# Kernel optimization log

Hardware: AMD Instinct MI355X
Metric: run time of the kernel (lower is better)

## Reference

```python
import jax, jax.numpy as jnp
import numpy as np

S, B, H = 4096, 64, 256
D = 2.0
SIGMA = D / 2.0


def setup_inputs() -> dict:
    key = jax.random.key(0)
    ks = jax.random.split(key, 7)
    return {
        "e": jax.random.normal(ks[0], (S, B, H), dtype=jnp.float32),
        "d": jax.random.normal(ks[1], (1, B, H), dtype=jnp.float32),
        "W_a": jax.random.normal(ks[2], (H, H), dtype=jnp.float32) / np.sqrt(H),
        "W_p": jax.random.normal(ks[3], (H, H), dtype=jnp.float32) / np.sqrt(H),
        "v_p": jax.random.normal(ks[4], (H, 1), dtype=jnp.float32) / np.sqrt(H),
        "lin_w": jax.random.normal(ks[5], (H, 2 * H), dtype=jnp.float32) / np.sqrt(2 * H),
        "lin_b": jax.random.normal(ks[6], (H,), dtype=jnp.float32) * 0.01,
    }


def reference(e, d, W_a, W_p, v_p, lin_w, lin_b):
    s = e.shape[0]
    # alignment: scores over source positions, softmax along S (dim 0 in torch)
    scores = jnp.sum((d @ W_a) * e, axis=2)          # [S, B]
    a = jax.nn.softmax(scores, axis=0)               # [S, B]
    # predictive position gating (Luong local-p attention)
    h = jnp.tanh(d[0] @ W_p)                         # [B, H]
    p_center = jax.nn.sigmoid((h @ v_p)[:, 0])[None, :] * s   # [1, B]
    pos = jnp.arange(s, dtype=e.dtype)[:, None]      # [S, 1]
    diff = p_center - pos                            # [S, B]
    mask = (jnp.abs(diff) <= D).astype(e.dtype)
    p = jnp.exp(-(diff * diff) / (2.0 * SIGMA * SIGMA)) * mask  # [S, B]
    w = a * p                                        # [S, B]
    context = jnp.einsum('sbh,sb->bh', e, w)[None]   # [1, B, H]
    x = jnp.concatenate([context, d], axis=2)        # [1, B, 2H]
    out = jax.nn.relu(x @ lin_w.T + lin_b)           # dropout = identity (eval)
    return out, w
```

## Files before the change

### kernel.cpp

```cpp
#include <hip/hip_runtime.h>
#include <math.h>

constexpr int S_ = 4096;
constexpr int B_ = 64;
constexpr int H_ = 256;
constexpr int NCH = 16;
constexpr int ROWS = S_ / NCH;
constexpr float SHIFT = 60.0f;


__global__ __launch_bounds__(256) void kMain(const float* __restrict__ e,
                                             const float* __restrict__ d,
                                             const float* __restrict__ W_a,
                                             float* __restrict__ dW,
                                             float* __restrict__ lpart,
                                             float* __restrict__ w_out) {
  const int bid = blockIdx.x;
  const int b = bid & 63;
  const int c = bid >> 6;
  const int t = threadIdx.x;
  const int w = t >> 6;
  const int lane = t & 63;

  __shared__ float4 part[4][64];
  __shared__ float4 dw4[64];
  __shared__ float lred[64];

  {
    const float* db = d + b * H_;
    const float4* Wa4 = (const float4*)W_a;
    float4 acc = make_float4(0.f, 0.f, 0.f, 0.f);
#pragma unroll 8
    for (int i = 0; i < 64; ++i) {
      const int k = w * 64 + i;
      const float dv = db[k];
      const float4 wa = Wa4[k * 64 + lane];
      acc.x = fmaf(dv, wa.x, acc.x);
      acc.y = fmaf(dv, wa.y, acc.y);
      acc.z = fmaf(dv, wa.z, acc.z);
      acc.w = fmaf(dv, wa.w, acc.w);
    }
    part[w][lane] = acc;
    __syncthreads();
    if (t < 64) {
      float4 a0 = part[0][t], a1 = part[1][t], a2 = part[2][t], a3 = part[3][t];
      float4 r = make_float4(a0.x + a1.x + a2.x + a3.x,
                             a0.y + a1.y + a2.y + a3.y,
                             a0.z + a1.z + a2.z + a3.z,
                             a0.w + a1.w + a2.w + a3.w);
      dw4[t] = r;
      if (c == 0) ((float4*)(dW + b * H_))[t] = r;
    }
    __syncthreads();
  }

  const int rr = lane >> 2;
  const int sub = lane & 3;
  float4 wreg[16];
#pragma unroll
  for (int j = 0; j < 16; ++j) wreg[j] = dw4[sub + 4 * j];

  float lsum = 0.f;
#pragma unroll 1
  for (int p = 0; p < 4; ++p) {
    const int s = c * ROWS + p * 64 + w * 16 + rr;
    const float4* erow = (const float4*)(e + ((size_t)s * B_ + b) * H_);
    float acc = 0.f;
#pragma unroll
    for (int half = 0; half < 2; ++half) {
      float4 ev[8];
#pragma unroll
      for (int j = 0; j < 8; ++j) ev[j] = erow[sub + 4 * (half * 8 + j)];
#pragma unroll
      for (int j = 0; j < 8; ++j) {
        const float4 wv = wreg[half * 8 + j];
        acc = fmaf(ev[j].x, wv.x, fmaf(ev[j].y, wv.y,
              fmaf(ev[j].z, wv.z, fmaf(ev[j].w, wv.w, acc))));
      }
    }
    acc += __shfl_xor(acc, 1, 64);
    acc += __shfl_xor(acc, 2, 64);
    if (sub == 0) lsum += expf(acc - SHIFT);
  }
  if (sub == 0) lred[w * 16 + rr] = lsum;
  __syncthreads();
  if (t < 64) {
    float v = lred[t];
#pragma unroll
    for (int off = 32; off > 0; off >>= 1) v += __shfl_xor(v, off, 64);
    if (t == 0) lpart[b * NCH + c] = v;
  }
  w_out[bid * 256 + t] = 0.f;
}

__global__ __launch_bounds__(1024) void kD(const float* __restrict__ e,
                                           const float* __restrict__ d,
                                           const float* __restrict__ W_p,
                                           const float* __restrict__ v_p,
                                           const float* __restrict__ lin_w,
                                           const float* __restrict__ lin_b,
                                           const float* __restrict__ dW,
                                           const float* __restrict__ lpart,
                                           float* __restrict__ out,
                                           float* __restrict__ w_out) {
  const int b = blockIdx.x;
  const int t = threadIdx.x;
  __shared__ float red[1024];
  __shared__ float sstate[2];
  __shared__ float scW[8];
  __shared__ float wsh[8];
  __shared__ float xbuf[512];

  {
    const int h = t & 255, kc = t >> 8;
    const float* db = d + b * H_;
    float ap = 0.f;
#pragma unroll 8
    for (int k = kc * 64; k < kc * 64 + 64; ++k)
      ap = fmaf(db[k], W_p[k * H_ + h], ap);
    red[t] = ap;
    __syncthreads();
    if (t < 256) {
      float sp = red[t] + red[t + 256] + red[t + 512] + red[t + 768];
      red[t] = tanhf(sp) * v_p[t];
    }
    __syncthreads();
    for (int st = 128; st > 0; st >>= 1) {
      if (t < st) red[t] += red[t + st];
      __syncthreads();
    }
    if (t == 0) {
      sstate[0] = (float)S_ / (1.f + expf(-red[0]));
      float L = 0.f;
#pragma unroll
      for (int j = 0; j < NCH; ++j) L += lpart[b * NCH + j];
      sstate[1] = 1.f / L;
    }
    __syncthreads();
  }
  const float pcb = sstate[0];
  const float invL = sstate[1];
  const int s0 = max(0, (int)ceilf(pcb - 2.f));
  const int s1 = min(S_ - 1, (int)floorf(pcb + 2.f));
  const int nw = s1 - s0 + 1;

  if (t < nw * 64) {
    const int j = t >> 6, lane = t & 63;
    const float4 ev = ((const float4*)(e + ((size_t)(s0 + j) * B_ + b) * H_))[lane];
    const float4 wv = ((const float4*)(dW + b * H_))[lane];
    float p = ev.x * wv.x + ev.y * wv.y + ev.z * wv.z + ev.w * wv.w;
#pragma unroll
    for (int off = 32; off > 0; off >>= 1) p += __shfl_xor(p, off, 64);
    if (lane == 0) scW[j] = p;
  }
  __syncthreads();
  if (t < nw) {
    const int s = s0 + t;
    const float diff = pcb - (float)s;
    const float wv = expf(scW[t] - SHIFT) * invL * expf(-0.5f * diff * diff);
    wsh[t] = wv;
    w_out[(size_t)s * B_ + b] = wv;
  }
  __syncthreads();
  if (t < 256) {
    float ctx = 0.f;
    for (int j = 0; j < nw; ++j)
      ctx = fmaf(wsh[j], e[((size_t)(s0 + j) * B_ + b) * H_ + t], ctx);
    xbuf[t] = ctx;
    xbuf[256 + t] = d[b * H_ + t];
  }
  __syncthreads();
  const int h = t >> 2, prt = t & 3;
  const float4* lw = (const float4*)(lin_w + h * 2 * H_) + prt * 32;
  const float4* xv = (const float4*)xbuf + prt * 32;
  float acc = 0.f;
#pragma unroll 8
  for (int k = 0; k < 32; ++k) {
    float4 a4 = lw[k], b4 = xv[k];
    acc += a4.x * b4.x + a4.y * b4.y + a4.z * b4.z + a4.w * b4.w;
  }
  red[t] = acc;
  __syncthreads();
  if (t < 256) {
    float r = red[4 * t] + red[4 * t + 1] + red[4 * t + 2] + red[4 * t + 3] + lin_b[t];
    out[b * H_ + t] = fmaxf(r, 0.f);
  }
}

extern "C" void kernel_launch(void* const* d_in, const int* in_sizes, int n_in,
                              void* d_out, int out_size, void* d_ws, size_t ws_size,
                              hipStream_t stream) {
  const float* e     = (const float*)d_in[0];
  const float* dd    = (const float*)d_in[1];
  const float* W_a   = (const float*)d_in[2];
  const float* W_p   = (const float*)d_in[3];
  const float* v_p   = (const float*)d_in[4];
  const float* lin_w = (const float*)d_in[5];
  const float* lin_b = (const float*)d_in[6];

  float* out   = (float*)d_out;
  float* w_out = out + B_ * H_;

  float* ws    = (float*)d_ws;
  float* dW    = ws;
  float* lpart = ws + 16384;

  kMain<<<B_ * NCH, 256, 0, stream>>>(e, dd, W_a, dW, lpart, w_out);
  kD<<<B_, 1024, 0, stream>>>(e, dd, W_p, v_p, lin_w, lin_b, dW, lpart, out, w_out);
}
```

Before: 69.67 us.

## Fuse the two kernels with a last-block-done atomic counter per batch

Merges the tail kernel into the main kernel. Each block publishes its partial softmax sum and bumps a per-batch atomic counter, and the last of the 16 chunk blocks for a batch runs the position gating, context and output projection. This removes a second launch and the dW round-trip through global memory. In exchange the tail work runs on 256 threads instead of 1024, so the W_p and lin_w dot products become serial per thread. The counters are never reset, so the modulo-16 check depends on them starting at zero and counting up across calls.

```diff
diff --git a/kernel.cpp b/kernel.cpp
--- a/kernel.cpp
+++ b/kernel.cpp
@@ -9,12 +9,13 @@
 constexpr float SHIFT = 60.0f;
 
 
-__global__ __launch_bounds__(256) void kMain(const float* __restrict__ e,
-                                             const float* __restrict__ d,
-                                             const float* __restrict__ W_a,
-                                             float* __restrict__ dW,
-                                             float* __restrict__ lpart,
-                                             float* __restrict__ w_out) {
+__global__ __launch_bounds__(256) void kFull(
+    const float* __restrict__ e, const float* __restrict__ d,
+    const float* __restrict__ W_a, const float* __restrict__ W_p,
+    const float* __restrict__ v_p, const float* __restrict__ lin_w,
+    const float* __restrict__ lin_b, float* __restrict__ lpart,
+    unsigned int* __restrict__ counters, float* __restrict__ out,
+    float* __restrict__ w_out) {
   const int bid = blockIdx.x;
   const int b = bid & 63;
   const int c = bid >> 6;
@@ -25,6 +26,12 @@
   __shared__ float4 part[4][64];
   __shared__ float4 dw4[64];
   __shared__ float lred[64];
+  __shared__ unsigned int ordS;
+  __shared__ float red[256];
+  __shared__ float sst[2];
+  __shared__ float scW[8];
+  __shared__ float wsh[8];
+  __shared__ float xbuf[512];
 
   {
     const float* db = d + b * H_;
@@ -44,12 +51,10 @@
     __syncthreads();
     if (t < 64) {
       float4 a0 = part[0][t], a1 = part[1][t], a2 = part[2][t], a3 = part[3][t];
-      float4 r = make_float4(a0.x + a1.x + a2.x + a3.x,
-                             a0.y + a1.y + a2.y + a3.y,
-                             a0.z + a1.z + a2.z + a3.z,
-                             a0.w + a1.w + a2.w + a3.w);
-      dw4[t] = r;
-      if (c == 0) ((float4*)(dW + b * H_))[t] = r;
+      dw4[t] = make_float4(a0.x + a1.x + a2.x + a3.x,
+                           a0.y + a1.y + a2.y + a3.y,
+                           a0.z + a1.z + a2.z + a3.z,
+                           a0.w + a1.w + a2.w + a3.w);
     }
     __syncthreads();
   }
@@ -88,66 +93,47 @@
     float v = lred[t];
 #pragma unroll
     for (int off = 32; off > 0; off >>= 1) v += __shfl_xor(v, off, 64);
-    if (t == 0) lpart[b * NCH + c] = v;
+    if (t == 0) {
+      __hip_atomic_store(&lpart[b * 16 + c], v, __ATOMIC_RELEASE,
+                         __HIP_MEMORY_SCOPE_AGENT);
+      ordS = __hip_atomic_fetch_add(&counters[b * 32], 1u, __ATOMIC_ACQ_REL,
+                                    __HIP_MEMORY_SCOPE_AGENT);
+    }
   }
-  w_out[bid * 256 + t] = 0.f;
-}
+  __syncthreads();
+  if ((ordS & 15u) != 15u) return;
 
-__global__ __launch_bounds__(1024) void kD(const float* __restrict__ e,
-                                           const float* __restrict__ d,
-                                           const float* __restrict__ W_p,
-                                           const float* __restrict__ v_p,
-                                           const float* __restrict__ lin_w,
-                                           const float* __restrict__ lin_b,
-                                           const float* __restrict__ dW,
-                                           const float* __restrict__ lpart,
-                                           float* __restrict__ out,
-                                           float* __restrict__ w_out) {
-  const int b = blockIdx.x;
-  const int t = threadIdx.x;
-  __shared__ float red[1024];
-  __shared__ float sstate[2];
-  __shared__ float scW[8];
-  __shared__ float wsh[8];
-  __shared__ float xbuf[512];
-
+  if (t == 0) {
+    float L = 0.f;
+#pragma unroll
+    for (int j = 0; j < NCH; ++j)
+      L += __hip_atomic_load(&lpart[b * 16 + j], __ATOMIC_RELAXED,
+                             __HIP_MEMORY_SCOPE_AGENT);
+    sst[1] = 1.f / L;
+  }
   {
-    const int h = t & 255, kc = t >> 8;
     const float* db = d + b * H_;
     float ap = 0.f;
 #pragma unroll 8
-    for (int k = kc * 64; k < kc * 64 + 64; ++k)
-      ap = fmaf(db[k], W_p[k * H_ + h], ap);
-    red[t] = ap;
-    __syncthreads();
-    if (t < 256) {
-      float sp = red[t] + red[t + 256] + red[t + 512] + red[t + 768];
-      red[t] = tanhf(sp) * v_p[t];
-    }
-    __syncthreads();
-    for (int st = 128; st > 0; st >>= 1) {
-      if (t < st) red[t] += red[t + st];
-      __syncthreads();
-    }
-    if (t == 0) {
-      sstate[0] = (float)S_ / (1.f + expf(-red[0]));
-      float L = 0.f;
-#pragma unroll
-      for (int j = 0; j < NCH; ++j) L += lpart[b * NCH + j];
-      sstate[1] = 1.f / L;
-    }
+    for (int k = 0; k < H_; ++k) ap = fmaf(db[k], W_p[k * H_ + t], ap);
+    red[t] = tanhf(ap) * v_p[t];
+  }
+  __syncthreads();
+  for (int st = 128; st > 0; st >>= 1) {
+    if (t < st) red[t] += red[t + st];
     __syncthreads();
   }
-  const float pcb = sstate[0];
-  const float invL = sstate[1];
+  if (t == 0) sst[0] = (float)S_ / (1.f + expf(-red[0]));
+  __syncthreads();
+  const float pcb = sst[0];
+  const float invL = sst[1];
   const int s0 = max(0, (int)ceilf(pcb - 2.f));
   const int s1 = min(S_ - 1, (int)floorf(pcb + 2.f));
   const int nw = s1 - s0 + 1;
 
-  if (t < nw * 64) {
-    const int j = t >> 6, lane = t & 63;
+  for (int j = w; j < nw; j += 4) {
     const float4 ev = ((const float4*)(e + ((size_t)(s0 + j) * B_ + b) * H_))[lane];
-    const float4 wv = ((const float4*)(dW + b * H_))[lane];
+    const float4 wv = dw4[lane];
     float p = ev.x * wv.x + ev.y * wv.y + ev.z * wv.z + ev.w * wv.w;
 #pragma unroll
     for (int off = 32; off > 0; off >>= 1) p += __shfl_xor(p, off, 64);
@@ -157,12 +143,16 @@
   if (t < nw) {
     const int s = s0 + t;
     const float diff = pcb - (float)s;
-    const float wv = expf(scW[t] - SHIFT) * invL * expf(-0.5f * diff * diff);
-    wsh[t] = wv;
-    w_out[(size_t)s * B_ + b] = wv;
+    wsh[t] = expf(scW[t] - SHIFT) * invL * expf(-0.5f * diff * diff);
   }
   __syncthreads();
-  if (t < 256) {
+#pragma unroll
+  for (int i = 0; i < 16; ++i) {
+    const int s = t + i * 256;
+    const int j = s - s0;
+    w_out[(size_t)s * B_ + b] = (j >= 0 && j < nw) ? wsh[j] : 0.f;
+  }
+  {
     float ctx = 0.f;
     for (int j = 0; j < nw; ++j)
       ctx = fmaf(wsh[j], e[((size_t)(s0 + j) * B_ + b) * H_ + t], ctx);
@@ -170,20 +160,17 @@
     xbuf[256 + t] = d[b * H_ + t];
   }
   __syncthreads();
-  const int h = t >> 2, prt = t & 3;
-  const float4* lw = (const float4*)(lin_w + h * 2 * H_) + prt * 32;
-  const float4* xv = (const float4*)xbuf + prt * 32;
-  float acc = 0.f;
+  {
+    float acc = lin_b[t];
+    const float4* lw = (const float4*)(lin_w + t * 2 * H_);
+    const float4* xv = (const float4*)xbuf;
 #pragma unroll 8
-  for (int k = 0; k < 32; ++k) {
-    float4 a4 = lw[k], b4 = xv[k];
-    acc += a4.x * b4.x + a4.y * b4.y + a4.z * b4.z + a4.w * b4.w;
-  }
-  red[t] = acc;
-  __syncthreads();
-  if (t < 256) {
-    float r = red[4 * t] + red[4 * t + 1] + red[4 * t + 2] + red[4 * t + 3] + lin_b[t];
-    out[b * H_ + t] = fmaxf(r, 0.f);
+    for (int k = 0; k < 128; ++k) {
+      float4 a4 = lw[k];
+      float4 b4 = xv[k];
+      acc += a4.x * b4.x + a4.y * b4.y + a4.z * b4.z + a4.w * b4.w;
+    }
+    out[b * H_ + t] = fmaxf(acc, 0.f);
   }
 }
 
@@ -202,9 +189,9 @@
   float* w_out = out + B_ * H_;
 
   float* ws    = (float*)d_ws;
-  float* dW    = ws;
-  float* lpart = ws + 16384;
+  float* lpart = ws;
+  unsigned int* counters = (unsigned int*)(ws + 1024);
 
-  kMain<<<B_ * NCH, 256, 0, stream>>>(e, dd, W_a, dW, lpart, w_out);
-  kD<<<B_, 1024, 0, stream>>>(e, dd, W_p, v_p, lin_w, lin_b, dW, lpart, out, w_out);
+  kFull<<<B_ * NCH, 256, 0, stream>>>(e, dd, W_a, W_p, v_p, lin_w, lin_b,
+                                      lpart, counters, out, w_out);
 }
```

Result: slower. 136.7 us (+96.3%).
